# Optimization experiments

Hardware: AMD Instinct MI355X
Metric: run time of the kernel (lower is better)

The kernel has to match this reference:

```python
import jax, jax.numpy as jnp
import numpy as np

BSZ, D = 64, 65536
N_NODES, N_FEATS, EMBED_DIM = 1024, 256, 256


def setup_inputs() -> dict:
    key = jax.random.key(0)
    k1, k2, k3, k4, k5, k6 = jax.random.split(key, 6)
    flat_inputs = jax.random.normal(k1, (BSZ, D), dtype=jnp.float32)
    node_ids = jax.random.randint(k2, (BSZ, D), 0, N_NODES, dtype=jnp.int64 if jax.config.jax_enable_x64 else jnp.int32)
    feat_ids = jax.random.randint(k3, (BSZ, D), 0, N_FEATS, dtype=jnp.int64 if jax.config.jax_enable_x64 else jnp.int32)
    # Linear(n_feats -> embed_dim): W is (embed_dim, n_feats) like torch, plus bias.
    lim = 1.0 / np.sqrt(N_FEATS)
    W = jax.random.uniform(k4, (EMBED_DIM, N_FEATS), minval=-lim, maxval=lim, dtype=jnp.float32)
    b = jax.random.uniform(k5, (EMBED_DIM,), minval=-lim, maxval=lim, dtype=jnp.float32)
    global_emb = jax.random.normal(k6, (N_NODES, EMBED_DIM), dtype=jnp.float32)
    return {"flat_inputs": flat_inputs, "node_ids": node_ids, "feat_ids": feat_ids,
            "W": W, "b": b, "global_emb": global_emb}


def _expand(vals, node_ids, feat_ids, n_nodes, n_feats):
    # scatter-fill a dense (bsz, n_nodes, n_feats) tensor (zeros elsewhere)
    bsz, d = vals.shape
    batch_ids = jnp.broadcast_to(jnp.arange(bsz)[:, None], (bsz, d))
    out = jnp.zeros((bsz, n_nodes, n_feats), dtype=vals.dtype)
    return out.at[batch_ids.ravel(), node_ids.ravel(), feat_ids.ravel()].set(vals.ravel())


def reference(flat_inputs, node_ids, feat_ids, W, b, global_emb):
    obs_mat = _expand(flat_inputs, node_ids, feat_ids, N_NODES, N_FEATS)
    mask_mat = _expand(jnp.ones_like(flat_inputs), node_ids, feat_ids, N_NODES, N_FEATS)
    obs_counts = mask_mat.sum(-1, keepdims=True)            # (bsz, n_nodes, 1)
    obs_masked = jnp.nan_to_num((obs_mat * mask_mat) / obs_counts)
    missing_node_mask = obs_counts == 0
    # nodewise Linear + global embedding broadcast over batch
    embedded = jnp.einsum('bnf,ef->bne', obs_masked, W) + b + global_emb[None, :, :]
    return embedded, missing_node_mask
```

## Files before the change

### kernel.cpp

```cpp
#include <hip/hip_runtime.h>
#include <hip/hip_bf16.h>

#define BSZ    64
#define DLEN   65536
#define NNODES 1024
#define NFEATS 256
#define EDIM   256
#define NROWS  (BSZ * NNODES)

#define NRANGE  16
#define NBUCKET (BSZ * NRANGE)
#define LCAP    320
#define GCAP    4600
#define WPAD    268

typedef __bf16 bf16x8 __attribute__((ext_vector_type(8)));
typedef float  f32x4  __attribute__((ext_vector_type(4)));

__device__ __forceinline__ unsigned short f2bf(float x) {
  union { float f; unsigned u; } c; c.f = x;
  unsigned r = c.u + 0x7FFFu + ((c.u >> 16) & 1u);
  return (unsigned short)(r >> 16);
}

__global__ __launch_bounds__(256) void wconv_kernel(
    const float* __restrict__ W, unsigned short* __restrict__ Wb,
    unsigned* __restrict__ gcnt) {
  int i = (blockIdx.x * 256 + threadIdx.x) * 4;
  float4 w = *(const float4*)(W + i);
  ushort4 o;
  o.x = f2bf(w.x); o.y = f2bf(w.y); o.z = f2bf(w.z); o.w = f2bf(w.w);
  *(ushort4*)(Wb + i) = o;
  if (blockIdx.x == 0) ((uint4*)gcnt)[threadIdx.x] = make_uint4(0u, 0u, 0u, 0u);
}

__global__ __launch_bounds__(512, 6) void bucket_kernel(
    const float* __restrict__ x, const int* __restrict__ nid,
    const int* __restrict__ fid, unsigned* __restrict__ gcnt,
    uint2* __restrict__ gbuf) {
  __shared__ uint2 lbuf[NRANGE][LCAP];
  __shared__ unsigned lcnt[NRANGE];
  __shared__ unsigned lbase[NRANGE];

  const int t = threadIdx.x;
  if (t < NRANGE) lcnt[t] = 0;
  __syncthreads();

  const int b = blockIdx.x >> 4;
  const int base = blockIdx.x * 4096;

#pragma unroll
  for (int k = 0; k < 2; ++k) {
    int i = base + (k * 512 + t) * 4;
    float4 xv = *(const float4*)(x + i);
    int4   nv = *(const int4*)(nid + i);
    int4   fv = *(const int4*)(fid + i);
    int   nd[4] = {nv.x, nv.y, nv.z, nv.w};
    int   ft[4] = {fv.x, fv.y, fv.z, fv.w};
    float vl[4] = {xv.x, xv.y, xv.z, xv.w};
#pragma unroll
    for (int j = 0; j < 4; ++j) {
      int d = (i + j) & 0xFFFF;
      unsigned pack = (((unsigned)(d + 1)) << 15) | ((unsigned)f2bf(vl[j]) >> 1);
      int r = nd[j] >> 6;
      unsigned row = (unsigned)(nd[j] & 63);
      uint2 rec;
      rec.x = pack;
      rec.y = (row << 16) | (row * WPAD + (unsigned)ft[j]);
      unsigned li = atomicAdd(&lcnt[r], 1u);
      if (li < LCAP) {
        lbuf[r][li] = rec;
      } else {
        unsigned gi = atomicAdd(&gcnt[b * NRANGE + r], 1u);
        if (gi < GCAP) gbuf[(size_t)(b * NRANGE + r) * GCAP + gi] = rec;
      }
    }
  }
  __syncthreads();

  if (t < NRANGE) {
    unsigned n = lcnt[t]; if (n > LCAP) n = LCAP;
    lcnt[t] = n;
    lbase[t] = atomicAdd(&gcnt[b * NRANGE + t], n);
  }
  __syncthreads();

  for (int r = 0; r < NRANGE; ++r) {
    unsigned n  = lcnt[r];
    unsigned bs = lbase[r];
    uint2* dst = gbuf + (size_t)(b * NRANGE + r) * GCAP;
    for (unsigned j = t; j < n; j += 512) {
      unsigned gi = bs + j;
      if (gi < GCAP) dst[gi] = lbuf[r][j];
    }
  }
}

__global__ __launch_bounds__(512, 4) void fused_kernel(
    const unsigned* __restrict__ gcnt, const uint2* __restrict__ gbuf,
    const unsigned short* __restrict__ Wb, const float* __restrict__ bias,
    const float* __restrict__ gemb,
    float* __restrict__ out_emb, float* __restrict__ out_mask) {
  __shared__ __align__(16) unsigned win[64 * WPAD];
  __shared__ int counts[64];
  __shared__ float scl[64];

  const int t = threadIdx.x;
  const int g = blockIdx.x;
  const int row0 = g * 64;
  const int nb = (g & 15) * 64;

  uint4* wz = (uint4*)win;
  for (int j = t; j < (64 * WPAD) / 4; j += 512) wz[j] = make_uint4(0u, 0u, 0u, 0u);
  if (t < 64) counts[t] = 0;
  __syncthreads();

  int cn = (int)gcnt[g]; if (cn > GCAP) cn = GCAP;
  const uint2* bk = gbuf + (size_t)g * GCAP;
  const uint4* bk4 = (const uint4*)bk;
  int np = cn >> 1;
  for (int j = t; j < np; j += 512) {
    uint4 rr = bk4[j];
    unsigned old0 = atomicMax(&win[rr.y & 0xFFFFu], rr.x);
    if (old0 == 0u) atomicAdd(&counts[rr.y >> 16], 1);
    unsigned old1 = atomicMax(&win[rr.w & 0xFFFFu], rr.z);
    if (old1 == 0u) atomicAdd(&counts[rr.w >> 16], 1);
  }
  if ((cn & 1) && t == 0) {
    uint2 rec = bk[cn - 1];
    unsigned old = atomicMax(&win[rec.y & 0xFFFFu], rec.x);
    if (old == 0u) atomicAdd(&counts[rec.y >> 16], 1);
  }
  __syncthreads();

  if (t < 64) {
    int c = counts[t];
    scl[t] = c ? 1.0f / (float)c : 0.0f;
    out_mask[row0 + t] = c ? 0.0f : 1.0f;
  }

  const int wv   = t >> 6;
  const int lane = t & 63;
  const int cl   = lane & 15;
  const int q    = lane >> 4;
  const int col0 = wv * 32;

  f32x4 acc[4][2];
#pragma unroll
  for (int mt = 0; mt < 4; ++mt)
#pragma unroll
    for (int nt = 0; nt < 2; ++nt) acc[mt][nt] = (f32x4)(0.0f);

#pragma unroll
  for (int ks = 0; ks < 8; ++ks) {
    bf16x8 bfr[2];
#pragma unroll
    for (int nt = 0; nt < 2; ++nt) {
      const uint4* wp = (const uint4*)(Wb + (size_t)(col0 + nt * 16 + cl) * NFEATS + ks * 32 + q * 8);
      bfr[nt] = __builtin_bit_cast(bf16x8, *wp);
    }
#pragma unroll
    for (int mt = 0; mt < 4; ++mt) {
      const uint4* ap = (const uint4*)&win[(mt * 16 + cl) * WPAD + ks * 32 + q * 8];
      uint4 lo = ap[0], hi = ap[1];
      uint4 pk;
      pk.x = ((lo.x & 0x7FFFu) << 1) | ((lo.y & 0x7FFFu) << 17);
      pk.y = ((lo.z & 0x7FFFu) << 1) | ((lo.w & 0x7FFFu) << 17);
      pk.z = ((hi.x & 0x7FFFu) << 1) | ((hi.y & 0x7FFFu) << 17);
      pk.w = ((hi.z & 0x7FFFu) << 1) | ((hi.w & 0x7FFFu) << 17);
      bf16x8 afr = __builtin_bit_cast(bf16x8, pk);
#pragma unroll
      for (int nt = 0; nt < 2; ++nt)
        acc[mt][nt] = __builtin_amdgcn_mfma_f32_16x16x32_bf16(afr, bfr[nt], acc[mt][nt], 0, 0, 0);
    }
  }
  __syncthreads();

#pragma unroll
  for (int nt = 0; nt < 2; ++nt) {
    int col = col0 + nt * 16 + cl;
    float bv = bias[col];
#pragma unroll
    for (int mt = 0; mt < 4; ++mt) {
#pragma unroll
      for (int r2 = 0; r2 < 4; ++r2) {
        int row = mt * 16 + q * 4 + r2;
        float o = acc[mt][nt][r2] * scl[row] + bv + gemb[(size_t)(nb + row) * EDIM + col];
        out_emb[(size_t)(row0 + row) * EDIM + col] = o;
      }
    }
  }
}

extern "C" void kernel_launch(void* const* d_in, const int* in_sizes, int n_in,
                              void* d_out, int out_size, void* d_ws, size_t ws_size,
                              hipStream_t stream) {
  const float* x    = (const float*)d_in[0];
  const int*   nid  = (const int*)d_in[1];
  const int*   fid  = (const int*)d_in[2];
  const float* W    = (const float*)d_in[3];
  const float* bias = (const float*)d_in[4];
  const float* gemb = (const float*)d_in[5];

  float* out_emb  = (float*)d_out;
  float* out_mask = out_emb + (size_t)NROWS * EDIM;

  unsigned* gcnt = (unsigned*)d_ws;
  uint2* gbuf = (uint2*)((char*)d_ws + 8192);
  unsigned short* Wb = (unsigned short*)((char*)d_ws + 8192 + (size_t)NBUCKET * GCAP * sizeof(uint2));

  wconv_kernel<<<64, 256, 0, stream>>>(W, Wb, gcnt);
  bucket_kernel<<<(BSZ * DLEN) / 4096, 512, 0, stream>>>(x, nid, fid, gcnt, gbuf);
  fused_kernel<<<NBUCKET, 512, 0, stream>>>(gcnt, gbuf, Wb, bias, gemb, out_emb, out_mask);
}
```

Baseline: 148.3 us.

## Split buckets to 32-node ranges with compact SoA pack/slot records

Halves the node range per bucket (32 nodes instead of 64), doubling the number of fused-kernel blocks and halving each block's shared-memory window. Bucket records shrink from 8 bytes to 6 bytes by storing a 16-bit slot (node-in-range, feature) in a separate array, and the LDS index is recomputed on the consumer side. Occupancy hints are swapped between the two kernels. The intent is to cut scatter traffic and raise parallelism and occupancy in the GEMM stage. The cost is more atomic-counter contention across more buckets, smaller per-block MFMA tiles, and extra index arithmetic.

```diff
diff --git a/kernel.cpp b/kernel.cpp
--- a/kernel.cpp
+++ b/kernel.cpp
@@ -8,10 +8,10 @@
 #define EDIM   256
 #define NROWS  (BSZ * NNODES)
 
-#define NRANGE  16
+#define NRANGE  32
 #define NBUCKET (BSZ * NRANGE)
-#define LCAP    320
-#define GCAP    4600
+#define LCAP    192
+#define GCAP    2400
 #define WPAD    268
 
 typedef __bf16 bf16x8 __attribute__((ext_vector_type(8)));
@@ -31,14 +31,18 @@
   ushort4 o;
   o.x = f2bf(w.x); o.y = f2bf(w.y); o.z = f2bf(w.z); o.w = f2bf(w.w);
   *(ushort4*)(Wb + i) = o;
-  if (blockIdx.x == 0) ((uint4*)gcnt)[threadIdx.x] = make_uint4(0u, 0u, 0u, 0u);
-}
-
-__global__ __launch_bounds__(512, 6) void bucket_kernel(
+  if (blockIdx.x == 0) {
+    ((uint4*)gcnt)[threadIdx.x] = make_uint4(0u, 0u, 0u, 0u);
+    ((uint4*)gcnt)[threadIdx.x + 256] = make_uint4(0u, 0u, 0u, 0u);
+  }
+}
+
+__global__ __launch_bounds__(512, 4) void bucket_kernel(
     const float* __restrict__ x, const int* __restrict__ nid,
     const int* __restrict__ fid, unsigned* __restrict__ gcnt,
-    uint2* __restrict__ gbuf) {
-  __shared__ uint2 lbuf[NRANGE][LCAP];
+    unsigned* __restrict__ gpack, unsigned short* __restrict__ gslot) {
+  __shared__ unsigned lpack[NRANGE][LCAP];
+  __shared__ unsigned short lslot[NRANGE][LCAP];
   __shared__ unsigned lcnt[NRANGE];
   __shared__ unsigned lbase[NRANGE];
 
@@ -62,17 +66,18 @@
     for (int j = 0; j < 4; ++j) {
       int d = (i + j) & 0xFFFF;
       unsigned pack = (((unsigned)(d + 1)) << 15) | ((unsigned)f2bf(vl[j]) >> 1);
-      int r = nd[j] >> 6;
-      unsigned row = (unsigned)(nd[j] & 63);
-      uint2 rec;
-      rec.x = pack;
-      rec.y = (row << 16) | (row * WPAD + (unsigned)ft[j]);
+      int r = nd[j] >> 5;
+      unsigned short slot = (unsigned short)(((nd[j] & 31) << 8) | ft[j]);
       unsigned li = atomicAdd(&lcnt[r], 1u);
       if (li < LCAP) {
-        lbuf[r][li] = rec;
+        lpack[r][li] = pack;
+        lslot[r][li] = slot;
       } else {
         unsigned gi = atomicAdd(&gcnt[b * NRANGE + r], 1u);
-        if (gi < GCAP) gbuf[(size_t)(b * NRANGE + r) * GCAP + gi] = rec;
+        if (gi < GCAP) {
+          gpack[(size_t)(b * NRANGE + r) * GCAP + gi] = pack;
+          gslot[(size_t)(b * NRANGE + r) * GCAP + gi] = slot;
+        }
       }
     }
   }
@@ -88,52 +93,59 @@
   for (int r = 0; r < NRANGE; ++r) {
     unsigned n  = lcnt[r];
     unsigned bs = lbase[r];
-    uint2* dst = gbuf + (size_t)(b * NRANGE + r) * GCAP;
+    unsigned* dp = gpack + (size_t)(b * NRANGE + r) * GCAP;
+    unsigned short* ds = gslot + (size_t)(b * NRANGE + r) * GCAP;
     for (unsigned j = t; j < n; j += 512) {
       unsigned gi = bs + j;
-      if (gi < GCAP) dst[gi] = lbuf[r][j];
-    }
-  }
-}
-
-__global__ __launch_bounds__(512, 4) void fused_kernel(
-    const unsigned* __restrict__ gcnt, const uint2* __restrict__ gbuf,
+      if (gi < GCAP) { dp[gi] = lpack[r][j]; ds[gi] = lslot[r][j]; }
+    }
+  }
+}
+
+__global__ __launch_bounds__(512, 6) void fused_kernel(
+    const unsigned* __restrict__ gcnt, const unsigned* __restrict__ gpack,
+    const unsigned short* __restrict__ gslot,
     const unsigned short* __restrict__ Wb, const float* __restrict__ bias,
     const float* __restrict__ gemb,
     float* __restrict__ out_emb, float* __restrict__ out_mask) {
-  __shared__ __align__(16) unsigned win[64 * WPAD];
-  __shared__ int counts[64];
-  __shared__ float scl[64];
+  __shared__ __align__(16) unsigned win[32 * WPAD];
+  __shared__ int counts[32];
+  __shared__ float scl[32];
 
   const int t = threadIdx.x;
   const int g = blockIdx.x;
-  const int row0 = g * 64;
-  const int nb = (g & 15) * 64;
+  const int row0 = g * 32;
+  const int nb = (g & 31) * 32;
 
   uint4* wz = (uint4*)win;
-  for (int j = t; j < (64 * WPAD) / 4; j += 512) wz[j] = make_uint4(0u, 0u, 0u, 0u);
-  if (t < 64) counts[t] = 0;
+  for (int j = t; j < (32 * WPAD) / 4; j += 512) wz[j] = make_uint4(0u, 0u, 0u, 0u);
+  if (t < 32) counts[t] = 0;
   __syncthreads();
 
   int cn = (int)gcnt[g]; if (cn > GCAP) cn = GCAP;
-  const uint2* bk = gbuf + (size_t)g * GCAP;
-  const uint4* bk4 = (const uint4*)bk;
+  const unsigned* pkb = gpack + (size_t)g * GCAP;
+  const unsigned short* slb = gslot + (size_t)g * GCAP;
   int np = cn >> 1;
   for (int j = t; j < np; j += 512) {
-    uint4 rr = bk4[j];
-    unsigned old0 = atomicMax(&win[rr.y & 0xFFFFu], rr.x);
-    if (old0 == 0u) atomicAdd(&counts[rr.y >> 16], 1);
-    unsigned old1 = atomicMax(&win[rr.w & 0xFFFFu], rr.z);
-    if (old1 == 0u) atomicAdd(&counts[rr.w >> 16], 1);
+    uint2 pp = ((const uint2*)pkb)[j];
+    unsigned ss = ((const unsigned*)slb)[j];
+    unsigned s0 = ss & 0xFFFFu, s1 = ss >> 16;
+    unsigned i0 = (s0 >> 8) * WPAD + (s0 & 255u);
+    unsigned i1 = (s1 >> 8) * WPAD + (s1 & 255u);
+    unsigned old0 = atomicMax(&win[i0], pp.x);
+    if (old0 == 0u) atomicAdd(&counts[s0 >> 8], 1);
+    unsigned old1 = atomicMax(&win[i1], pp.y);
+    if (old1 == 0u) atomicAdd(&counts[s1 >> 8], 1);
   }
   if ((cn & 1) && t == 0) {
-    uint2 rec = bk[cn - 1];
-    unsigned old = atomicMax(&win[rec.y & 0xFFFFu], rec.x);
-    if (old == 0u) atomicAdd(&counts[rec.y >> 16], 1);
-  }
-  __syncthreads();
-
-  if (t < 64) {
+    unsigned pack = pkb[cn - 1];
+    unsigned s0 = slb[cn - 1];
+    unsigned old = atomicMax(&win[(s0 >> 8) * WPAD + (s0 & 255u)], pack);
+    if (old == 0u) atomicAdd(&counts[s0 >> 8], 1);
+  }
+  __syncthreads();
+
+  if (t < 32) {
     int c = counts[t];
     scl[t] = c ? 1.0f / (float)c : 0.0f;
     out_mask[row0 + t] = c ? 0.0f : 1.0f;
@@ -145,9 +157,9 @@
   const int q    = lane >> 4;
   const int col0 = wv * 32;
 
-  f32x4 acc[4][2];
-#pragma unroll
-  for (int mt = 0; mt < 4; ++mt)
+  f32x4 acc[2][2];
+#pragma unroll
+  for (int mt = 0; mt < 2; ++mt)
 #pragma unroll
     for (int nt = 0; nt < 2; ++nt) acc[mt][nt] = (f32x4)(0.0f);
 
@@ -160,7 +172,7 @@
       bfr[nt] = __builtin_bit_cast(bf16x8, *wp);
     }
 #pragma unroll
-    for (int mt = 0; mt < 4; ++mt) {
+    for (int mt = 0; mt < 2; ++mt) {
       const uint4* ap = (const uint4*)&win[(mt * 16 + cl) * WPAD + ks * 32 + q * 8];
       uint4 lo = ap[0], hi = ap[1];
       uint4 pk;
@@ -181,7 +193,7 @@
     int col = col0 + nt * 16 + cl;
     float bv = bias[col];
 #pragma unroll
-    for (int mt = 0; mt < 4; ++mt) {
+    for (int mt = 0; mt < 2; ++mt) {
 #pragma unroll
       for (int r2 = 0; r2 < 4; ++r2) {
         int row = mt * 16 + q * 4 + r2;
@@ -206,10 +218,11 @@
   float* out_mask = out_emb + (size_t)NROWS * EDIM;
 
   unsigned* gcnt = (unsigned*)d_ws;
-  uint2* gbuf = (uint2*)((char*)d_ws + 8192);
-  unsigned short* Wb = (unsigned short*)((char*)d_ws + 8192 + (size_t)NBUCKET * GCAP * sizeof(uint2));
+  unsigned* gpack = (unsigned*)((char*)d_ws + 16384);
+  unsigned short* gslot = (unsigned short*)((char*)gpack + (size_t)NBUCKET * GCAP * sizeof(unsigned));
+  unsigned short* Wb = (unsigned short*)((char*)gslot + (size_t)NBUCKET * GCAP * sizeof(unsigned short));
 
   wconv_kernel<<<64, 256, 0, stream>>>(W, Wb, gcnt);
-  bucket_kernel<<<(BSZ * DLEN) / 4096, 512, 0, stream>>>(x, nid, fid, gcnt, gbuf);
-  fused_kernel<<<NBUCKET, 512, 0, stream>>>(gcnt, gbuf, Wb, bias, gemb, out_emb, out_mask);
-}
+  bucket_kernel<<<(BSZ * DLEN) / 4096, 512, 0, stream>>>(x, nid, fid, gcnt, gpack, gslot);
+  fused_kernel<<<NBUCKET, 512, 0, stream>>>(gcnt, gpack, gslot, Wb, bias, gemb, out_emb, out_mask);
+}
```

Measured after the change: 155.2 us. 4.7% more time.
